# Performance work log

Hardware: AMD Instinct MI355X
Metric: run time of the kernel (lower is better)

Reference implementation:

```python
import jax, jax.numpy as jnp
import numpy as np

B, S, D_IN, D_OUT, H = 2, 2048, 1024, 1024, 16
HD = D_OUT // H

def setup_inputs() -> dict:
    key = jax.random.key(0)
    ks = jax.random.split(key, 6)
    sc_in = 1.0 / np.sqrt(D_IN)
    sc_out = 1.0 / np.sqrt(D_OUT)
    return {
        "x": jax.random.normal(ks[0], (B, S, D_IN), dtype=jnp.float32),
        "Wq": jax.random.uniform(ks[1], (D_IN, D_OUT), jnp.float32, -sc_in, sc_in),
        "Wk": jax.random.uniform(ks[2], (D_IN, D_OUT), jnp.float32, -sc_in, sc_in),
        "Wv": jax.random.uniform(ks[3], (D_IN, D_OUT), jnp.float32, -sc_in, sc_in),
        "Wo": jax.random.uniform(ks[4], (D_OUT, D_OUT), jnp.float32, -sc_out, sc_out),
        "bo": jax.random.uniform(ks[5], (D_OUT,), jnp.float32, -sc_out, sc_out),
    }

def reference(x, Wq, Wk, Wv, Wo, bo):
    b, s, _ = x.shape
    # QKV projections (no bias), split heads -> [b, h, s, hd]
    q = (x @ Wq).reshape(b, s, H, HD).transpose(0, 2, 1, 3)
    k = (x @ Wk).reshape(b, s, H, HD).transpose(0, 2, 1, 3)
    v = (x @ Wv).reshape(b, s, H, HD).transpose(0, 2, 1, 3)
    scores = jnp.einsum('bhqd,bhkd->bhqk', q, k)
    causal = jnp.triu(jnp.ones((s, s), dtype=bool), k=1)
    scores = jnp.where(causal, -jnp.inf, scores)
    w = jax.nn.softmax(scores / np.sqrt(HD), axis=-1)  # dropout p=0.0 -> identity
    ctx = jnp.einsum('bhqk,bhkd->bhqd', w, v)
    ctx = ctx.transpose(0, 2, 1, 3).reshape(b, s, D_OUT)
    return ctx @ Wo + bo
```

## Files before the change

### kernel.cpp

```cpp
#include <hip/hip_runtime.h>
#include <stdint.h>

typedef unsigned short u16;
typedef __attribute__((ext_vector_type(8))) short short8;
typedef __attribute__((ext_vector_type(4))) float floatx4;
typedef __attribute__((ext_vector_type(4))) u16 ushort4v;

typedef __attribute__((address_space(1))) const uint32_t gu32;
typedef __attribute__((address_space(3))) uint32_t lu32;

#define MFMA(a, b, c) __builtin_amdgcn_mfma_f32_16x16x32_bf16((a), (b), (c), 0, 0, 0)

__device__ __forceinline__ u16 f2bf(float f) {
    union { float f; uint32_t u; } x; x.f = f;
    uint32_t u = x.u;
    u += 0x7fffu + ((u >> 16) & 1u);
    return (u16)(u >> 16);
}

__device__ __forceinline__ uint32_t cvtpk_bf16(float lo, float hi) {
    uint32_t r;
    asm("v_cvt_pk_bf16_f32 %0, %1, %2" : "=v"(r) : "v"(lo), "v"(hi));
    return r;
}

__device__ __forceinline__ float fexp2(float x) {
#if defined(__has_builtin)
#if __has_builtin(__builtin_amdgcn_exp2f)
    return __builtin_amdgcn_exp2f(x);
#else
    return exp2f(x);
#endif
#else
    return exp2f(x);
#endif
}

__device__ __forceinline__ void async16(u16* lds, const u16* g) {
    __builtin_amdgcn_global_load_lds((gu32*)g, (lu32*)lds, 16, 0, 0);
}

#define KV8(buf, row, byteInRow) \
    (*(short8*)((char*)(buf) + (((row) << 7) + ((byteInRow) ^ (((row) & 7) << 4)))))

#define Q_SCALE_LOG2E 0.18033688011112042f

__global__ __launch_bounds__(256) void prep_kernel(
    const float* __restrict__ x,
    const float* __restrict__ W0, const float* __restrict__ W1,
    const float* __restrict__ W2, const float* __restrict__ W3,
    u16* __restrict__ WT, u16* __restrict__ Xbf)
{
    const int z = blockIdx.z;
    const int tx = threadIdx.x, ty = threadIdx.y;
    if (z == 4) {
        const int bid = blockIdx.y * 32 + blockIdx.x;
        const int t = ty * 32 + tx;
        const size_t base = ((size_t)bid * 256 + t) * 16;
        const float* xf = x + base;
        short8 v0, v1;
#pragma unroll
        for (int j = 0; j < 8; j++) v0[j] = (short)f2bf(xf[j]);
#pragma unroll
        for (int j = 0; j < 8; j++) v1[j] = (short)f2bf(xf[8 + j]);
        *(short8*)&Xbf[base] = v0;
        *(short8*)&Xbf[base + 8] = v1;
        return;
    }
    __shared__ u16 tile[32][33];
    const float* W = (z == 0) ? W0 : (z == 1) ? W1 : (z == 2) ? W2 : W3;
    u16* dst = WT + (size_t)z * 1024 * 1024;
    const int n0 = blockIdx.x * 32, k0 = blockIdx.y * 32;
#pragma unroll
    for (int i = 0; i < 4; i++)
        tile[ty + i * 8][tx] = f2bf(W[(size_t)(k0 + ty + i * 8) * 1024 + n0 + tx]);
    __syncthreads();
#pragma unroll
    for (int i = 0; i < 4; i++)
        dst[(size_t)(n0 + ty + i * 8) * 1024 + k0 + tx] = tile[tx][ty + i * 8];
}

#define GSTAGE64(buf, gptr, kk) do { \
    _Pragma("unroll") \
    for (int i_ = 0; i_ < 4; i_++) \
        async16((buf) + wave * 512 + i_ * 2048, (gptr) + (kk) + (size_t)i_ * 32 * 1024); \
} while (0)

#define GFRAG64(buf, base, ks, fr) \
    (*(const short8*)&(buf)[((base) + (fr) * 16 + lrow) * 64 + ((((ks) * 4 + lquad) ^ (lrow & 7)) * 8)])

#define GCOMPUTE64() do { \
    _Pragma("unroll") \
    for (int ks = 0; ks < 2; ks++) { \
        short8 af[4], bfv[4]; \
        _Pragma("unroll") \
        for (int mt = 0; mt < 4; mt++) af[mt] = GFRAG64(As, wr, ks, mt); \
        _Pragma("unroll") \
        for (int nt = 0; nt < 4; nt++) bfv[nt] = GFRAG64(Bs, wc, ks, nt); \
        _Pragma("unroll") \
        for (int mt = 0; mt < 4; mt++) \
            _Pragma("unroll") \
            for (int nt = 0; nt < 4; nt++) \
                acc[mt][nt] = MFMA(af[mt], bfv[nt], acc[mt][nt]); \
    } \
} while (0)

#define GEMM_K_LOOP64() do { \
    for (int kk = 0; kk < 1024; kk += 64) { \
        __syncthreads(); \
        GSTAGE64(As, gA, kk); \
        GSTAGE64(Bs, gB, kk); \
        __syncthreads(); \
        GCOMPUTE64(); \
    } \
} while (0)

__global__ __launch_bounds__(256) void gemm_qkv_kernel(
    const u16* __restrict__ X, const u16* __restrict__ WT,
    u16* __restrict__ Q, u16* __restrict__ Kout, u16* __restrict__ VT)
{
    __shared__ __align__(16) u16 As[128 * 64];
    __shared__ __align__(16) u16 Bs[128 * 64];
    const int bid = blockIdx.x;
    const int xcd = bid & 7;
    const int idx = bid >> 3;
    const int mat = idx >> 5;
    const int rr  = (idx >> 3) & 3;
    const int nn  = idx & 7;
    const int m0 = (xcd * 4 + rr) * 128;
    const int n0 = nn * 128;
    const u16* BW = WT + (size_t)mat * 1024 * 1024;
    const int tid = threadIdx.x;
    const int wave = tid >> 6, lane = tid & 63;
    const int lrow = lane & 15, lquad = lane >> 4;
    const int wr = (wave >> 1) * 64, wc = (wave & 1) * 64;

    const int stg_r = tid >> 3;
    const int stg_c = ((tid & 7) ^ ((tid >> 3) & 7)) * 8;
    const u16* gA = &X[(size_t)(m0 + stg_r) * 1024 + stg_c];
    const u16* gB = &BW[(size_t)(n0 + stg_r) * 1024 + stg_c];

    floatx4 acc[4][4];
#pragma unroll
    for (int mt = 0; mt < 4; mt++)
#pragma unroll
        for (int nt = 0; nt < 4; nt++) acc[mt][nt] = (floatx4){0.f, 0.f, 0.f, 0.f};

    GEMM_K_LOOP64();

    const float qs = (mat == 0) ? Q_SCALE_LOG2E : 1.0f;
#pragma unroll
    for (int mt = 0; mt < 4; mt++) {
        const int gm = m0 + wr + mt * 16 + lquad * 4;
        const int b_ = gm >> 11;
        const int s  = gm & 2047;
#pragma unroll
        for (int nt = 0; nt < 4; nt++) {
            const int gn = n0 + wc + nt * 16 + lrow;
            const int h = gn >> 6, hd = gn & 63;
            const int bh = b_ * 16 + h;
            if (mat == 2) {
                ushort4v v;
#pragma unroll
                for (int i = 0; i < 4; i++) v[i] = f2bf(acc[mt][nt][i]);
                *(ushort4v*)&VT[((size_t)bh * 64 + hd) * 2048 + s] = v;
            } else {
                u16* dst = (mat == 0) ? Q : Kout;
#pragma unroll
                for (int i = 0; i < 4; i++)
                    dst[((size_t)bh * 2048 + s + i) * 64 + hd] = f2bf(acc[mt][nt][i] * qs);
            }
        }
    }
}

__global__ __launch_bounds__(256, 4) void attn_kernel(
    const u16* __restrict__ Q, const u16* __restrict__ Kk,
    const u16* __restrict__ VT, u16* __restrict__ ctx)
{
    __shared__ __align__(16) u16 Ks[64 * 64];
    __shared__ __align__(16) u16 Vs[64 * 64];
    __shared__ __align__(16) u16 P[4][16][80];
    const int tid = threadIdx.x, wave = tid >> 6, lane = tid & 63;
    const int lrow = lane & 15, lquad = lane >> 4;
    const float NEGINF = -__builtin_inff();

    const int bh = blockIdx.x & 31;
    const int g = blockIdx.x >> 5;
    const int qb = (g < 16) ? (31 - g) : (g - 16);
    const int ntiles = qb + 1;
    const int q0 = qb * 64 + wave * 16;

    const u16* Qb = Q  + (size_t)bh * 2048 * 64;
    const u16* Kb = Kk + (size_t)bh * 2048 * 64;
    const u16* Vb = VT + (size_t)bh * 64 * 2048;

    const short8 qf0 = *(const short8*)&Qb[(size_t)(q0 + lrow) * 64 + lquad * 8];
    const short8 qf1 = *(const short8*)&Qb[(size_t)(q0 + lrow) * 64 + 32 + lquad * 8];

    const int myq = q0 + lrow;
    float m_s = NEGINF, l_s = 0.f;
    floatx4 o[4];
#pragma unroll
    for (int i = 0; i < 4; i++) o[i] = (floatx4){0.f, 0.f, 0.f, 0.f};

    const int r0 = tid >> 3, r1 = r0 + 32;
    const int ce = (tid & 7) * 8;
    const int cb = (tid & 7) * 16;

    short8 kreg0 = *(const short8*)&Kb[(size_t)r0 * 64 + ce];
    short8 kreg1 = *(const short8*)&Kb[(size_t)r1 * 64 + ce];
    short8 vreg0 = *(const short8*)&Vb[(size_t)r0 * 2048 + ce];
    short8 vreg1 = *(const short8*)&Vb[(size_t)r1 * 2048 + ce];

    for (int kt = 0; kt < ntiles; kt++) {
        __syncthreads();
        KV8(Ks, r0, cb) = kreg0;
        KV8(Ks, r1, cb) = kreg1;
        KV8(Vs, r0, cb) = vreg0;
        KV8(Vs, r1, cb) = vreg1;
        if (kt + 1 < ntiles) {
            kreg0 = *(const short8*)&Kb[(size_t)((kt + 1) * 64 + r0) * 64 + ce];
            kreg1 = *(const short8*)&Kb[(size_t)((kt + 1) * 64 + r1) * 64 + ce];
            vreg0 = *(const short8*)&Vb[(size_t)r0 * 2048 + (kt + 1) * 64 + ce];
            vreg1 = *(const short8*)&Vb[(size_t)r1 * 2048 + (kt + 1) * 64 + ce];
        }
        __syncthreads();

        floatx4 s[4];
#pragma unroll
        for (int nt = 0; nt < 4; nt++) {
            const short8 kf0 = KV8(Ks, nt * 16 + lrow, lquad * 16);
            const short8 kf1 = KV8(Ks, nt * 16 + lrow, 64 + lquad * 16);
            floatx4 a = (floatx4){0.f, 0.f, 0.f, 0.f};
            a = MFMA(kf0, qf0, a);
            a = MFMA(kf1, qf1, a);
            s[nt] = a;
        }

        if (kt == ntiles - 1) {
#pragma unroll
            for (int nt = 0; nt < 4; nt++)
#pragma unroll
                for (int i = 0; i < 4; i++)
                    if (kt * 64 + nt * 16 + lquad * 4 + i > myq) s[nt][i] = NEGINF;
        }

        float mx = NEGINF;
#pragma unroll
        for (int nt = 0; nt < 4; nt++)
            mx = fmaxf(mx, fmaxf(fmaxf(s[nt][0], s[nt][1]),
                                 fmaxf(s[nt][2], s[nt][3])));
        mx = fmaxf(mx, __shfl_xor(mx, 16));
        mx = fmaxf(mx, __shfl_xor(mx, 32));

        if (!__all(mx <= m_s + 8.0f)) {
            const float mnew = fmaxf(m_s, mx);
            const float alpha = fexp2(m_s - mnew);
            m_s = mnew;
            l_s *= alpha;
#pragma unroll
            for (int ht = 0; ht < 4; ht++)
#pragma unroll
                for (int i = 0; i < 4; i++) o[ht][i] *= alpha;
        }

        float sum = 0.f;
#pragma unroll
        for (int nt = 0; nt < 4; nt++)
#pragma unroll
            for (int i = 0; i < 4; i++) {
                const float pv = fexp2(s[nt][i] - m_s);
                s[nt][i] = pv;
                sum += pv;
            }
        sum += __shfl_xor(sum, 16);
        sum += __shfl_xor(sum, 32);
        l_s += sum;

#pragma unroll
        for (int nt = 0; nt < 4; nt++) {
            uint2 pk;
            pk.x = cvtpk_bf16(s[nt][0], s[nt][1]);
            pk.y = cvtpk_bf16(s[nt][2], s[nt][3]);
            *(uint2*)&P[wave][lrow][nt * 16 + lquad * 4] = pk;
        }
#pragma unroll
        for (int st = 0; st < 2; st++) {
            const short8 pf = *(const short8*)&P[wave][lrow][st * 32 + lquad * 8];
#pragma unroll
            for (int ht = 0; ht < 4; ht++) {
                const short8 vf = KV8(Vs, ht * 16 + lrow, st * 64 + lquad * 16);
                o[ht] = MFMA(vf, pf, o[ht]);
            }
        }
    }

    const int b_ = bh >> 4, h_ = bh & 15;
    const float inv_l = 1.0f / l_s;
#pragma unroll
    for (int ht = 0; ht < 4; ht++) {
        uint2 pk;
        pk.x = cvtpk_bf16(o[ht][0] * inv_l, o[ht][1] * inv_l);
        pk.y = cvtpk_bf16(o[ht][2] * inv_l, o[ht][3] * inv_l);
        *(uint2*)&ctx[((size_t)(b_ * 2048 + q0 + lrow)) * 1024 + h_ * 64 + ht * 16 + lquad * 4] = pk;
    }
}

__global__ __launch_bounds__(256) void gemm_out_kernel(
    const u16* __restrict__ X, const u16* __restrict__ WT,
    const float* __restrict__ bias, float* __restrict__ out)
{
    __shared__ __align__(16) u16 As[128 * 64];
    __shared__ __align__(16) u16 Bs[128 * 64];
    const int bid = blockIdx.x;
    const int xcd = bid & 7;
    const int idx = bid >> 3;
    const int rr  = idx >> 3;
    const int nn  = idx & 7;
    const int m0 = (xcd * 4 + rr) * 128;
    const int n0 = nn * 128;
    const int tid = threadIdx.x;
    const int wave = tid >> 6, lane = tid & 63;
    const int lrow = lane & 15, lquad = lane >> 4;
    const int wr = (wave >> 1) * 64, wc = (wave & 1) * 64;

    const int stg_r = tid >> 3;
    const int stg_c = ((tid & 7) ^ ((tid >> 3) & 7)) * 8;
    const u16* gA = &X[(size_t)(m0 + stg_r) * 1024 + stg_c];
    const u16* gB = &WT[(size_t)(n0 + stg_r) * 1024 + stg_c];

    floatx4 acc[4][4];
#pragma unroll
    for (int mt = 0; mt < 4; mt++)
#pragma unroll
        for (int nt = 0; nt < 4; nt++) acc[mt][nt] = (floatx4){0.f, 0.f, 0.f, 0.f};

    GEMM_K_LOOP64();

#pragma unroll
    for (int mt = 0; mt < 4; mt++) {
        const int gm = m0 + wr + mt * 16 + lquad * 4;
#pragma unroll
        for (int nt = 0; nt < 4; nt++) {
            const int gn = n0 + wc + nt * 16 + lrow;
            const float bv = bias[gn];
#pragma unroll
            for (int i = 0; i < 4; i++)
                out[(size_t)(gm + i) * 1024 + gn] = acc[mt][nt][i] + bv;
        }
    }
}

extern "C" void kernel_launch(void* const* d_in, const int* in_sizes, int n_in,
                              void* d_out, int out_size, void* d_ws, size_t ws_size,
                              hipStream_t stream) {
    u16* ws = (u16*)d_ws + 64;

    const size_t MB1 = 1024 * 1024;
    u16* WT   = ws;
    u16* Qw   = ws + 4 * MB1;
    u16* Kw   = ws + 8 * MB1;
    u16* VTw  = ws + 12 * MB1;
    u16* ctxw = ws + 16 * MB1;
    u16* Xbf  = ws + 20 * MB1;

    prep_kernel<<<dim3(32, 32, 5), dim3(32, 8), 0, stream>>>(
        (const float*)d_in[0], (const float*)d_in[1], (const float*)d_in[2],
        (const float*)d_in[3], (const float*)d_in[4], WT, Xbf);
    gemm_qkv_kernel<<<768, 256, 0, stream>>>(Xbf, WT, Qw, Kw, VTw);
    attn_kernel<<<1024, 256, 0, stream>>>(Qw, Kw, VTw, ctxw);
    gemm_out_kernel<<<256, 256, 0, stream>>>(ctxw, WT + 3 * MB1, (const float*)d_in[5], (float*)d_out);
}
```

Before: 180.7 us.

## Load GEMM A and attention V fragments directly from global, double-buffer shared tiles

The GEMM kernels no longer stage the A operand through shared memory. Each wave loads its A fragments straight from global into registers, while the B tile is double-buffered in LDS with async copies overlapping compute. The attention kernel likewise reads V fragments directly from global into registers instead of via LDS, and ping-pongs the K tile between two LDS buffers to drop one barrier per iteration. This cuts LDS traffic and synchronisation, at the cost of uncoalesced, redundant global reads of A across waves and more register pressure.

```diff
diff --git a/kernel.cpp b/kernel.cpp
--- a/kernel.cpp
+++ b/kernel.cpp
@@ -80,38 +80,50 @@
         dst[(size_t)(n0 + ty + i * 8) * 1024 + k0 + tx] = tile[tx][ty + i * 8];
 }
 
-#define GSTAGE64(buf, gptr, kk) do { \
+#define GSTAGE_B(buf, kk) do { \
     _Pragma("unroll") \
     for (int i_ = 0; i_ < 4; i_++) \
-        async16((buf) + wave * 512 + i_ * 2048, (gptr) + (kk) + (size_t)i_ * 32 * 1024); \
+        async16((buf) + wave * 512 + i_ * 2048, gB + (kk) + (size_t)i_ * 32 * 1024); \
 } while (0)
 
 #define GFRAG64(buf, base, ks, fr) \
     (*(const short8*)&(buf)[((base) + (fr) * 16 + lrow) * 64 + ((((ks) * 4 + lquad) ^ (lrow & 7)) * 8)])
 
-#define GCOMPUTE64() do { \
+#define LDA_REGS(kk) do { \
+    _Pragma("unroll") \
+    for (int ks = 0; ks < 2; ks++) \
+        _Pragma("unroll") \
+        for (int mt = 0; mt < 4; mt++) \
+            areg[ks][mt] = *(const short8*)&gAr[(size_t)mt * 16 * 1024 + (kk) + ks * 32]; \
+} while (0)
+
+#define GCOMPUTE_RB(bbuf) do { \
     _Pragma("unroll") \
     for (int ks = 0; ks < 2; ks++) { \
-        short8 af[4], bfv[4]; \
+        short8 bfv[4]; \
         _Pragma("unroll") \
-        for (int mt = 0; mt < 4; mt++) af[mt] = GFRAG64(As, wr, ks, mt); \
-        _Pragma("unroll") \
-        for (int nt = 0; nt < 4; nt++) bfv[nt] = GFRAG64(Bs, wc, ks, nt); \
+        for (int nt = 0; nt < 4; nt++) bfv[nt] = GFRAG64(bbuf, wc, ks, nt); \
         _Pragma("unroll") \
         for (int mt = 0; mt < 4; mt++) \
             _Pragma("unroll") \
             for (int nt = 0; nt < 4; nt++) \
-                acc[mt][nt] = MFMA(af[mt], bfv[nt], acc[mt][nt]); \
+                acc[mt][nt] = MFMA(areg[ks][mt], bfv[nt], acc[mt][nt]); \
     } \
 } while (0)
 
-#define GEMM_K_LOOP64() do { \
-    for (int kk = 0; kk < 1024; kk += 64) { \
+#define GEMM_LOOP_RB() do { \
+    GSTAGE_B(Bs0, 0); \
+    __syncthreads(); \
+    for (int t8 = 0; t8 < 8; ++t8) { \
+        const int kk = t8 * 128; \
+        GSTAGE_B(Bs1, kk + 64); \
+        LDA_REGS(kk); \
+        GCOMPUTE_RB(Bs0); \
         __syncthreads(); \
-        GSTAGE64(As, gA, kk); \
-        GSTAGE64(Bs, gB, kk); \
+        if (t8 < 7) GSTAGE_B(Bs0, kk + 128); \
+        LDA_REGS(kk + 64); \
+        GCOMPUTE_RB(Bs1); \
         __syncthreads(); \
-        GCOMPUTE64(); \
     } \
 } while (0)
 
@@ -119,8 +131,8 @@
     const u16* __restrict__ X, const u16* __restrict__ WT,
     u16* __restrict__ Q, u16* __restrict__ Kout, u16* __restrict__ VT)
 {
-    __shared__ __align__(16) u16 As[128 * 64];
-    __shared__ __align__(16) u16 Bs[128 * 64];
+    __shared__ __align__(16) u16 Bs0[128 * 64];
+    __shared__ __align__(16) u16 Bs1[128 * 64];
     const int bid = blockIdx.x;
     const int xcd = bid & 7;
     const int idx = bid >> 3;
@@ -137,16 +149,17 @@
 
     const int stg_r = tid >> 3;
     const int stg_c = ((tid & 7) ^ ((tid >> 3) & 7)) * 8;
-    const u16* gA = &X[(size_t)(m0 + stg_r) * 1024 + stg_c];
     const u16* gB = &BW[(size_t)(n0 + stg_r) * 1024 + stg_c];
-
+    const u16* gAr = &X[(size_t)(m0 + wr + lrow) * 1024 + lquad * 8];
+
+    short8 areg[2][4];
     floatx4 acc[4][4];
 #pragma unroll
     for (int mt = 0; mt < 4; mt++)
 #pragma unroll
         for (int nt = 0; nt < 4; nt++) acc[mt][nt] = (floatx4){0.f, 0.f, 0.f, 0.f};
 
-    GEMM_K_LOOP64();
+    GEMM_LOOP_RB();
 
     const float qs = (mat == 0) ? Q_SCALE_LOG2E : 1.0f;
 #pragma unroll
@@ -178,8 +191,7 @@
     const u16* __restrict__ Q, const u16* __restrict__ Kk,
     const u16* __restrict__ VT, u16* __restrict__ ctx)
 {
-    __shared__ __align__(16) u16 Ks[64 * 64];
-    __shared__ __align__(16) u16 Vs[64 * 64];
+    __shared__ __align__(16) u16 Ks[2][64 * 64];
     __shared__ __align__(16) u16 P[4][16][80];
     const int tid = threadIdx.x, wave = tid >> 6, lane = tid & 63;
     const int lrow = lane & 15, lquad = lane >> 4;
@@ -210,33 +222,35 @@
 
     short8 kreg0 = *(const short8*)&Kb[(size_t)r0 * 64 + ce];
     short8 kreg1 = *(const short8*)&Kb[(size_t)r1 * 64 + ce];
-    short8 vreg0 = *(const short8*)&Vb[(size_t)r0 * 2048 + ce];
-    short8 vreg1 = *(const short8*)&Vb[(size_t)r1 * 2048 + ce];
 
     for (int kt = 0; kt < ntiles; kt++) {
-        __syncthreads();
-        KV8(Ks, r0, cb) = kreg0;
-        KV8(Ks, r1, cb) = kreg1;
-        KV8(Vs, r0, cb) = vreg0;
-        KV8(Vs, r1, cb) = vreg1;
+        u16* Kc = Ks[kt & 1];
+        KV8(Kc, r0, cb) = kreg0;
+        KV8(Kc, r1, cb) = kreg1;
         if (kt + 1 < ntiles) {
             kreg0 = *(const short8*)&Kb[(size_t)((kt + 1) * 64 + r0) * 64 + ce];
             kreg1 = *(const short8*)&Kb[(size_t)((kt + 1) * 64 + r1) * 64 + ce];
-            vreg0 = *(const short8*)&Vb[(size_t)r0 * 2048 + (kt + 1) * 64 + ce];
-            vreg1 = *(const short8*)&Vb[(size_t)r1 * 2048 + (kt + 1) * 64 + ce];
         }
         __syncthreads();
 
         floatx4 s[4];
 #pragma unroll
         for (int nt = 0; nt < 4; nt++) {
-            const short8 kf0 = KV8(Ks, nt * 16 + lrow, lquad * 16);
-            const short8 kf1 = KV8(Ks, nt * 16 + lrow, 64 + lquad * 16);
+            const short8 kf0 = KV8(Kc, nt * 16 + lrow, lquad * 16);
+            const short8 kf1 = KV8(Kc, nt * 16 + lrow, 64 + lquad * 16);
             floatx4 a = (floatx4){0.f, 0.f, 0.f, 0.f};
             a = MFMA(kf0, qf0, a);
             a = MFMA(kf1, qf1, a);
             s[nt] = a;
         }
+
+        short8 vf0[4], vf1[4];
+#pragma unroll
+        for (int ht = 0; ht < 4; ht++)
+            vf0[ht] = *(const short8*)&Vb[(size_t)(ht * 16 + lrow) * 2048 + kt * 64 + lquad * 8];
+#pragma unroll
+        for (int ht = 0; ht < 4; ht++)
+            vf1[ht] = *(const short8*)&Vb[(size_t)(ht * 16 + lrow) * 2048 + kt * 64 + 32 + lquad * 8];
 
         if (kt == ntiles - 1) {
 #pragma unroll
@@ -285,14 +299,13 @@
             pk.y = cvtpk_bf16(s[nt][2], s[nt][3]);
             *(uint2*)&P[wave][lrow][nt * 16 + lquad * 4] = pk;
         }
-#pragma unroll
-        for (int st = 0; st < 2; st++) {
-            const short8 pf = *(const short8*)&P[wave][lrow][st * 32 + lquad * 8];
-#pragma unroll
-            for (int ht = 0; ht < 4; ht++) {
-                const short8 vf = KV8(Vs, ht * 16 + lrow, st * 64 + lquad * 16);
-                o[ht] = MFMA(vf, pf, o[ht]);
-            }
+        {
+            const short8 pf0 = *(const short8*)&P[wave][lrow][lquad * 8];
+#pragma unroll
+            for (int ht = 0; ht < 4; ht++) o[ht] = MFMA(vf0[ht], pf0, o[ht]);
+            const short8 pf1 = *(const short8*)&P[wave][lrow][32 + lquad * 8];
+#pragma unroll
+            for (int ht = 0; ht < 4; ht++) o[ht] = MFMA(vf1[ht], pf1, o[ht]);
         }
     }
 
@@ -311,8 +324,8 @@
     const u16* __restrict__ X, const u16* __restrict__ WT,
     const float* __restrict__ bias, float* __restrict__ out)
 {
-    __shared__ __align__(16) u16 As[128 * 64];
-    __shared__ __align__(16) u16 Bs[128 * 64];
+    __shared__ __align__(16) u16 Bs0[128 * 64];
+    __shared__ __align__(16) u16 Bs1[128 * 64];
     const int bid = blockIdx.x;
     const int xcd = bid & 7;
     const int idx = bid >> 3;
@@ -327,16 +340,17 @@
 
     const int stg_r = tid >> 3;
     const int stg_c = ((tid & 7) ^ ((tid >> 3) & 7)) * 8;
-    const u16* gA = &X[(size_t)(m0 + stg_r) * 1024 + stg_c];
     const u16* gB = &WT[(size_t)(n0 + stg_r) * 1024 + stg_c];
-
+    const u16* gAr = &X[(size_t)(m0 + wr + lrow) * 1024 + lquad * 8];
+
+    short8 areg[2][4];
     floatx4 acc[4][4];
 #pragma unroll
     for (int mt = 0; mt < 4; mt++)
 #pragma unroll
         for (int nt = 0; nt < 4; nt++) acc[mt][nt] = (floatx4){0.f, 0.f, 0.f, 0.f};
 
-    GEMM_K_LOOP64();
+    GEMM_LOOP_RB();
 
 #pragma unroll
     for (int mt = 0; mt < 4; mt++) {
```

New measurement: 239.5 us. 32.5% more time.
